# Kernel tuning notes

Hardware: AMD Instinct MI355X
Metric: run time of the kernel (lower is better)

## Reference

```python
import jax, jax.numpy as jnp
import numpy as np

B, T, D = 2, 1024, 1024
E, H, TOPK = 32, 256, 4
S, HS = 2, H * TOPK  # shared experts, shared hidden dim


def setup_inputs() -> dict:
    key = jax.random.key(0)
    ks = jax.random.split(key, 10)
    sc = 0.02
    return {
        "x": jax.random.normal(ks[0], (B, T, D), dtype=jnp.float32),
        "Wr": jax.random.normal(ks[1], (E, D), dtype=jnp.float32) * sc,
        "router_bias": jnp.zeros((E,), dtype=jnp.float32),
        "Wg": jax.random.normal(ks[2], (E, H, D), dtype=jnp.float32) * sc,
        "Wu": jax.random.normal(ks[3], (E, H, D), dtype=jnp.float32) * sc,
        "Wd": jax.random.normal(ks[4], (E, D, H), dtype=jnp.float32) * sc,
        "Sg": jax.random.normal(ks[5], (S, HS, D), dtype=jnp.float32) * sc,
        "Su": jax.random.normal(ks[6], (S, HS, D), dtype=jnp.float32) * sc,
        "Sd": jax.random.normal(ks[7], (S, D, HS), dtype=jnp.float32) * sc,
    }


def reference(x, Wr, router_bias, Wg, Wu, Wd, Sg, Su, Sd):
    Bx, Tx, Dx = x.shape
    flat = x.reshape(-1, Dx)                      # [N, D]
    N = flat.shape[0]

    # Router: softmax over raw logits, top-k selection on biased logits
    logits = flat @ Wr.T                          # [N, E]
    scores = jax.nn.softmax(logits, axis=-1)
    _, topk_idx = jax.lax.top_k(logits + router_bias, TOPK)   # [N, K]
    topk_scores = jnp.take_along_axis(scores, topk_idx, axis=-1)
    topk_scores = topk_scores / jnp.sum(topk_scores, axis=-1, keepdims=True)

    # Dense per-token per-expert combine weights (0 for unselected experts)
    cw = jnp.zeros((N, E), dtype=flat.dtype).at[
        jnp.arange(N)[:, None], topk_idx
    ].add(topk_scores)                            # [N, E]

    # Routed experts: SwiGLU applied per expert, zero-weighted if unselected
    g = jnp.einsum("nd,ehd->neh", flat, Wg)       # [N, E, H]
    u = jnp.einsum("nd,ehd->neh", flat, Wu)
    h = jax.nn.silu(g) * u
    hw = h * cw[:, :, None]                       # fold combine weight before down-proj
    out = jnp.einsum("neh,edh->nd", hw, Wd)       # [N, D]

    # Shared experts: always active, summed on top
    gs = jnp.einsum("nd,shd->nsh", flat, Sg)      # [N, S, HS]
    us = jnp.einsum("nd,shd->nsh", flat, Su)
    hs = jax.nn.silu(gs) * us
    out = out + jnp.einsum("nsh,sdh->nd", hs, Sd)

    return out.reshape(Bx, Tx, Dx)
```

## Files before the change

kernel.cpp:

```cpp
#include <hip/hip_runtime.h>
#include <hip/hip_bf16.h>


#define N_TOK 2048
#define DDIM 1024
#define NEXP 32
#define HDIM 256
#define TOPK 4
#define NSH 2
#define HSH 1024
#define CNTS 32
#define WMAX 160
#define WM2  96

typedef unsigned short us4 __attribute__((ext_vector_type(4)));
typedef unsigned short us8 __attribute__((ext_vector_type(8)));
typedef short bf16x8 __attribute__((ext_vector_type(8)));
typedef float f32x4 __attribute__((ext_vector_type(4)));

__device__ __forceinline__ unsigned short f2bf(float f) {
  union { float f; unsigned u; } v; v.f = f;
  unsigned r = v.u + 0x7fffu + ((v.u >> 16) & 1u);
  return (unsigned short)(r >> 16);
}
__device__ __forceinline__ float bf2f(unsigned short h) {
  union { unsigned u; float f; } v; v.u = ((unsigned)h) << 16; return v.f;
}
__device__ __forceinline__ uint2 cvt4u(float4 v) {
  union { __hip_bfloat162 b; unsigned u; } a, b2;
  a.b  = __float22bfloat162_rn(make_float2(v.x, v.y));
  b2.b = __float22bfloat162_rn(make_float2(v.z, v.w));
  return make_uint2(a.u, b2.u);
}

__device__ __forceinline__ void pipe_barrier() {
  asm volatile("s_waitcnt lgkmcnt(0)" ::: "memory");
  __builtin_amdgcn_s_barrier();
  __builtin_amdgcn_sched_barrier(0);
}

#define C_X4   524288L
#define C_WG4  2621440L
#define C_WU4  4718592L
#define C_WD4  6815744L
#define C_SG4  7340032L
#define C_SU4  7864320L
#define C_TOT4 8388608L
#define NCVT   16384

__global__ __launch_bounds__(256) void k_prep(const float* __restrict__ x,
                                              const float* __restrict__ Wr,
                                              const float* __restrict__ rb,
                                              const float* __restrict__ Wg,
                                              const float* __restrict__ Wu,
                                              const float* __restrict__ Wd,
                                              const float* __restrict__ Sg,
                                              const float* __restrict__ Su,
                                              const float* __restrict__ Sd,
                                              unsigned short* __restrict__ xb,
                                              unsigned short* __restrict__ Wgb,
                                              unsigned short* __restrict__ Wub,
                                              unsigned short* __restrict__ Wdb,
                                              unsigned short* __restrict__ Sgb,
                                              unsigned short* __restrict__ Sub,
                                              unsigned short* __restrict__ Sdb,
                                              int* __restrict__ cnt,
                                              int* __restrict__ ent,
                                              float* __restrict__ wgt) {
  __shared__ float sX[8 * 1024];
  __shared__ float sLog[8 * 32];
  int tid = threadIdx.x;
  if (blockIdx.x >= 256) {
    long base = (long)(blockIdx.x - 256) * 512;
    const float* s; unsigned short* d; long off;
    if (base < C_WG4) {
      if (base < C_X4)  { s = x;  d = xb;  off = base; }
      else              { s = Wg; d = Wgb; off = base - C_X4; }
    } else if (base < C_WD4) {
      if (base < C_WU4) { s = Wu; d = Wub; off = base - C_WG4; }
      else              { s = Wd; d = Wdb; off = base - C_WU4; }
    } else if (base < C_SU4) {
      if (base < C_SG4) { s = Sg; d = Sgb; off = base - C_WD4; }
      else              { s = Su; d = Sub; off = base - C_SG4; }
    } else              { s = Sd; d = Sdb; off = base - C_SU4; }
    long i0 = off + 2 * tid;
    float4 v0 = reinterpret_cast<const float4*>(s)[i0];
    float4 v1 = reinterpret_cast<const float4*>(s)[i0 + 1];
    uint2 a = cvt4u(v0), b = cvt4u(v1);
    uint4 o = make_uint4(a.x, a.y, b.x, b.y);
    reinterpret_cast<uint4*>(d)[(off >> 1) + tid] = o;
    return;
  }
  int blk = blockIdx.x;
  {
    const float4* xsrc = reinterpret_cast<const float4*>(x + (size_t)blk * 8 * 1024);
    float4* xdst = reinterpret_cast<float4*>(sX);
#pragma unroll
    for (int i = 0; i < 8; i++) xdst[tid + 256 * i] = xsrc[tid + 256 * i];
  }
  __syncthreads();
  int tloc = tid >> 5, e = tid & 31;
  const float4* wr4 = reinterpret_cast<const float4*>(Wr + (size_t)e * DDIM);
  const float* xr = sX + tloc * 1024;
  float acc = 0.f;
#pragma unroll 8
  for (int d4 = 0; d4 < 256; d4++) {
    float4 wv = wr4[d4];
    acc += xr[d4 * 4 + 0] * wv.x + xr[d4 * 4 + 1] * wv.y +
           xr[d4 * 4 + 2] * wv.z + xr[d4 * 4 + 3] * wv.w;
  }
  sLog[tloc * 32 + e] = acc;
  __syncthreads();
  if (tid < 8) {
    int tok = blk * 8 + tid;
    const float* lg = sLog + tid * 32;
    int usedmask = 0;
    int idx[TOPK]; float lv[TOPK];
#pragma unroll
    for (int k = 0; k < TOPK; k++) {
      float best = -3.4e38f; int bi = 0;
      for (int ee = 0; ee < NEXP; ee++) {
        if ((usedmask >> ee) & 1) continue;
        float v = lg[ee] + rb[ee];
        if (v > best) { best = v; bi = ee; }
      }
      usedmask |= 1 << bi; idx[k] = bi; lv[k] = lg[bi];
    }
    float m = fmaxf(fmaxf(lv[0], lv[1]), fmaxf(lv[2], lv[3]));
    float w[TOPK]; float ssum = 0.f;
#pragma unroll
    for (int k = 0; k < TOPK; k++) { w[k] = __expf(lv[k] - m); ssum += w[k]; }
    float inv = 1.f / ssum;
#pragma unroll
    for (int k = 0; k < TOPK; k++) {
      int ee = idx[k];
      int pos = atomicAdd(&cnt[ee * CNTS], 1);
      ent[ee * N_TOK + pos] = tok * TOPK + k;
      wgt[ee * N_TOK + pos] = w[k] * inv;
    }
  }
}

__global__ void k_plan(const int* __restrict__ cnt, int* __restrict__ wk, int* __restrict__ nwk,
                       int* __restrict__ wk2, int* __restrict__ nwk2) {
  if (threadIdx.x != 0) return;
  int w = 0, w2 = 0;
  for (int e = 0; e < NEXP; e++) {
    int ne = cnt[e * CNTS];
    int nt = (ne + 63) >> 6;
    for (int t = 0; t < nt; t++) wk[w++] = e | (t << 8);
    int nt2 = (ne + 127) >> 7;
    for (int t = 0; t < nt2; t++) wk2[w2++] = e | (t << 8);
  }
  nwk[0] = w;
  nwk2[0] = w2;
}

__global__ __launch_bounds__(512) void k_routed_gu(const unsigned short* __restrict__ xb,
                                                   const unsigned short* __restrict__ Wgb,
                                                   const unsigned short* __restrict__ Wub,
                                                   const int* __restrict__ cnt,
                                                   const int* __restrict__ ent,
                                                   const float* __restrict__ wgt,
                                                   unsigned short* __restrict__ hw,
                                                   const int* __restrict__ wk2,
                                                   const int* __restrict__ nwk2) {
  int widx = blockIdx.x;
  if (widx >= nwk2[0]) return;
  int item = wk2[widx];
  int e = item & 255, mt = item >> 8, ht = blockIdx.y;
  int ne = cnt[e * CNTS];
  __shared__ unsigned short sA[2][128 * 40];
  __shared__ unsigned short sB[2][128 * 40];
  __shared__ int sTok[128];
  __shared__ float sW[128];
  int tid = threadIdx.x, lane = tid & 63, wid = tid >> 6;
  int wm = wid >> 2, wn = wid & 3;
  if (tid < 128) {
    int pos = mt * 128 + tid;
    int p2 = min(pos, ne - 1);
    sTok[tid] = ent[e * N_TOK + p2];
    sW[tid] = (pos < ne) ? wgt[e * N_TOK + p2] : 0.f;
  }
  __syncthreads();

  int ar = tid >> 2, akc = tid & 3;
  const unsigned short* aSrc = xb + (size_t)(sTok[ar] >> 2) * DDIM + akc * 8;
  int aOff = ar * 40 + akc * 8;
  int br = tid >> 2, bkc = tid & 3;
  int sel = (br >> 4) & 1;
  int h = ht * 64 + ((br >> 5) << 4) + (br & 15);
  const unsigned short* bSrc = (sel ? Wub : Wgb) + (size_t)(e * HDIM + h) * DDIM + bkc * 8;
  int bOff = br * 40 + bkc * 8;

  us8 aReg = *reinterpret_cast<const us8*>(aSrc);
  us8 bReg = *reinterpret_cast<const us8*>(bSrc);

  f32x4 acc[4][2];
#pragma unroll
  for (int mf = 0; mf < 4; mf++)
#pragma unroll
    for (int nf = 0; nf < 2; nf++) acc[mf][nf] = {0.f, 0.f, 0.f, 0.f};

  int cur = 0;
  for (int step = 0; step < 32; ++step) {
    *reinterpret_cast<us8*>(&sA[cur][aOff]) = aReg;
    *reinterpret_cast<us8*>(&sB[cur][bOff]) = bReg;
    if (step < 31) {
      int k0 = (step + 1) * 32;
      aReg = *reinterpret_cast<const us8*>(aSrc + k0);
      bReg = *reinterpret_cast<const us8*>(bSrc + k0);
    }
    pipe_barrier();
    int ka = (lane >> 4) * 8;
    bf16x8 a[4];
#pragma unroll
    for (int mf = 0; mf < 4; mf++)
      a[mf] = *reinterpret_cast<const bf16x8*>(&sA[cur][(wm * 64 + mf * 16 + (lane & 15)) * 40 + ka]);
#pragma unroll
    for (int nf = 0; nf < 2; nf++) {
      bf16x8 b = *reinterpret_cast<const bf16x8*>(&sB[cur][(wn * 32 + nf * 16 + (lane & 15)) * 40 + ka]);
#pragma unroll
      for (int mf = 0; mf < 4; mf++)
        acc[mf][nf] = __builtin_amdgcn_mfma_f32_16x16x32_bf16(a[mf], b, acc[mf][nf], 0, 0, 0);
    }
    cur ^= 1;
  }
#pragma unroll
  for (int mf = 0; mf < 4; mf++) {
#pragma unroll
    for (int r = 0; r < 4; r++) {
      int tl = wm * 64 + mf * 16 + ((lane >> 4) << 2) + r;
      int pos = mt * 128 + tl;
      if (pos < ne) {
        float g = acc[mf][0][r], u = acc[mf][1][r];
        float hval = (g / (1.f + __expf(-g))) * u * sW[tl];
        int ts = sTok[tl];
        int hcol = ht * 64 + wn * 16 + (lane & 15);
        hw[(size_t)ts * HDIM + hcol] = f2bf(hval);
      }
    }
  }
}

__global__ __launch_bounds__(512) void k_routed_down(const unsigned short* __restrict__ hw,
                                                     const unsigned short* __restrict__ Wdb,
                                                     const int* __restrict__ cnt,
                                                     const int* __restrict__ ent,
                                                     unsigned short* __restrict__ Pslot,
                                                     const int* __restrict__ wk2,
                                                     const int* __restrict__ nwk2) {
  int widx = blockIdx.x;
  if (widx >= nwk2[0]) return;
  int item = wk2[widx];
  int e = item & 255, mt = item >> 8, dh = blockIdx.y;
  int ne = cnt[e * CNTS];
  __shared__ unsigned short sA[2][128 * 40];
  __shared__ unsigned short sB[2][128 * 40];
  __shared__ int sTok[128];
  int tid = threadIdx.x, lane = tid & 63, wid = tid >> 6;
  int wm = wid >> 2, wn = wid & 3;
  if (tid < 128) {
    int pos = mt * 128 + tid;
    int p2 = min(pos, ne - 1);
    sTok[tid] = ent[e * N_TOK + p2];
  }
  __syncthreads();

  int ar = tid >> 2, akc = tid & 3;
  const unsigned short* aSrc = hw + (size_t)sTok[ar] * HDIM + akc * 8;
  int aOff = ar * 40 + akc * 8;
  int br = tid >> 2, bkc = tid & 3;
  int d0 = dh * 128 + br;
  const unsigned short* bSrc = Wdb + (size_t)(e * DDIM + d0) * HDIM + bkc * 8;
  int bOff = br * 40 + bkc * 8;

  us8 aReg = *reinterpret_cast<const us8*>(aSrc);
  us8 bReg = *reinterpret_cast<const us8*>(bSrc);

  f32x4 acc[4][2];
#pragma unroll
  for (int mf = 0; mf < 4; mf++)
#pragma unroll
    for (int nf = 0; nf < 2; nf++) acc[mf][nf] = {0.f, 0.f, 0.f, 0.f};

  int cur = 0;
  for (int step = 0; step < 8; ++step) {
    *reinterpret_cast<us8*>(&sA[cur][aOff]) = aReg;
    *reinterpret_cast<us8*>(&sB[cur][bOff]) = bReg;
    if (step < 7) {
      int k0 = (step + 1) * 32;
      aReg = *reinterpret_cast<const us8*>(aSrc + k0);
      bReg = *reinterpret_cast<const us8*>(bSrc + k0);
    }
    pipe_barrier();
    int ka = (lane >> 4) * 8;
    bf16x8 a[4];
#pragma unroll
    for (int mf = 0; mf < 4; mf++)
      a[mf] = *reinterpret_cast<const bf16x8*>(&sA[cur][(wm * 64 + mf * 16 + (lane & 15)) * 40 + ka]);
#pragma unroll
    for (int nf = 0; nf < 2; nf++) {
      bf16x8 b = *reinterpret_cast<const bf16x8*>(&sB[cur][(wn * 32 + nf * 16 + (lane & 15)) * 40 + ka]);
#pragma unroll
      for (int mf = 0; mf < 4; mf++)
        acc[mf][nf] = __builtin_amdgcn_mfma_f32_16x16x32_bf16(a[mf], b, acc[mf][nf], 0, 0, 0);
    }
    cur ^= 1;
  }
#pragma unroll
  for (int mf = 0; mf < 4; mf++) {
#pragma unroll
    for (int nf = 0; nf < 2; nf++) {
#pragma unroll
      for (int r = 0; r < 4; r++) {
        int tl = wm * 64 + mf * 16 + ((lane >> 4) << 2) + r;
        int pos = mt * 128 + tl;
        if (pos < ne) {
          int ts = sTok[tl];
          int d = dh * 128 + wn * 32 + nf * 16 + (lane & 15);
          Pslot[(size_t)ts * DDIM + d] = f2bf(acc[mf][nf][r]);
        }
      }
    }
  }
}

__global__ __launch_bounds__(512) void k_shared_gu(const unsigned short* __restrict__ xb,
                                                   const unsigned short* __restrict__ Sgb,
                                                   const unsigned short* __restrict__ Sub,
                                                   unsigned short* __restrict__ hs) {
  int s = blockIdx.x >> 3, ht = blockIdx.x & 7;
  int mt = blockIdx.y;
  __shared__ unsigned short sA[2][128 * 40];
  __shared__ unsigned short sB[2][256 * 40];
  int tid = threadIdx.x, lane = tid & 63, wid = tid >> 6;
  int wm = wid >> 2, wn = wid & 3;

  int ar = tid >> 2, akc = tid & 3;
  const unsigned short* aSrc = xb + (size_t)(mt * 128 + ar) * DDIM + akc * 8;
  int aOff = ar * 40 + akc * 8;
  const unsigned short* bSrc[2];
  int bOff[2];
#pragma unroll
  for (int p = 0; p < 2; p++) {
    int c = tid + p * 512;
    int row = c >> 2, kc = c & 3;
    int sel = (row >> 4) & 1;
    int h = ht * 128 + ((row >> 5) << 4) + (row & 15);
    bSrc[p] = (sel ? Sub : Sgb) + (size_t)(s * HSH + h) * DDIM + kc * 8;
    bOff[p] = row * 40 + kc * 8;
  }

  us8 aReg = *reinterpret_cast<const us8*>(aSrc);
  us8 bReg[2];
#pragma unroll
  for (int p = 0; p < 2; p++) bReg[p] = *reinterpret_cast<const us8*>(bSrc[p]);

  f32x4 acc[4][4];
#pragma unroll
  for (int mf = 0; mf < 4; mf++)
#pragma unroll
    for (int nf = 0; nf < 4; nf++) acc[mf][nf] = {0.f, 0.f, 0.f, 0.f};

  int cur = 0;
  for (int step = 0; step < 32; ++step) {
    *reinterpret_cast<us8*>(&sA[cur][aOff]) = aReg;
#pragma unroll
    for (int p = 0; p < 2; p++) *reinterpret_cast<us8*>(&sB[cur][bOff[p]]) = bReg[p];
    if (step < 31) {
      int k0 = (step + 1) * 32;
      aReg = *reinterpret_cast<const us8*>(aSrc + k0);
#pragma unroll
      for (int p = 0; p < 2; p++) bReg[p] = *reinterpret_cast<const us8*>(bSrc[p] + k0);
    }
    pipe_barrier();
    int ka = (lane >> 4) * 8;
    bf16x8 a[4];
#pragma unroll
    for (int mf = 0; mf < 4; mf++)
      a[mf] = *reinterpret_cast<const bf16x8*>(&sA[cur][(wm * 64 + mf * 16 + (lane & 15)) * 40 + ka]);
#pragma unroll
    for (int nf = 0; nf < 4; nf++) {
      bf16x8 b = *reinterpret_cast<const bf16x8*>(&sB[cur][(wn * 64 + nf * 16 + (lane & 15)) * 40 + ka]);
#pragma unroll
      for (int mf = 0; mf < 4; mf++)
        acc[mf][nf] = __builtin_amdgcn_mfma_f32_16x16x32_bf16(a[mf], b, acc[mf][nf], 0, 0, 0);
    }
    cur ^= 1;
  }
#pragma unroll
  for (int mf = 0; mf < 4; mf++) {
#pragma unroll
    for (int t = 0; t < 2; t++) {
#pragma unroll
      for (int r = 0; r < 4; r++) {
        int tok = mt * 128 + wm * 64 + mf * 16 + ((lane >> 4) << 2) + r;
        float g = acc[mf][2 * t][r], u = acc[mf][2 * t + 1][r];
        float hval = (g / (1.f + __expf(-g))) * u;
        int h = ht * 128 + (wn * 2 + t) * 16 + (lane & 15);
        hs[(size_t)(tok * NSH + s) * HSH + h] = f2bf(hval);
      }
    }
  }
}

__global__ __launch_bounds__(512) void k_shared_down(const unsigned short* __restrict__ hs,
                                                     const unsigned short* __restrict__ Sdb,
                                                     unsigned short* __restrict__ Psh) {
  int dh = blockIdx.x >> 1, s = blockIdx.x & 1;
  int mt = blockIdx.y;
  __shared__ unsigned short sA[2][128 * 40];
  __shared__ unsigned short sB[2][128 * 40];
  int tid = threadIdx.x, lane = tid & 63, wid = tid >> 6;
  int wm = wid >> 2, wn = wid & 3;

  int ar = tid >> 2, akc = tid & 3;
  const unsigned short* aSrc = hs + (size_t)((mt * 128 + ar) * NSH + s) * HSH + akc * 8;
  int aOff = ar * 40 + akc * 8;
  int br = tid >> 2, bkc = tid & 3;
  const unsigned short* bSrc = Sdb + (size_t)(s * DDIM + dh * 128 + br) * HSH + bkc * 8;
  int bOff = br * 40 + bkc * 8;

  us8 aReg = *reinterpret_cast<const us8*>(aSrc);
  us8 bReg = *reinterpret_cast<const us8*>(bSrc);

  f32x4 acc[4][2];
#pragma unroll
  for (int mf = 0; mf < 4; mf++)
#pragma unroll
    for (int nf = 0; nf < 2; nf++) acc[mf][nf] = {0.f, 0.f, 0.f, 0.f};

  int cur = 0;
  for (int step = 0; step < 32; ++step) {
    *reinterpret_cast<us8*>(&sA[cur][aOff]) = aReg;
    *reinterpret_cast<us8*>(&sB[cur][bOff]) = bReg;
    if (step < 31) {
      int k0 = (step + 1) * 32;
      aReg = *reinterpret_cast<const us8*>(aSrc + k0);
      bReg = *reinterpret_cast<const us8*>(bSrc + k0);
    }
    pipe_barrier();
    int ka = (lane >> 4) * 8;
    bf16x8 a[4];
#pragma unroll
    for (int mf = 0; mf < 4; mf++)
      a[mf] = *reinterpret_cast<const bf16x8*>(&sA[cur][(wm * 64 + mf * 16 + (lane & 15)) * 40 + ka]);
#pragma unroll
    for (int nf = 0; nf < 2; nf++) {
      bf16x8 b = *reinterpret_cast<const bf16x8*>(&sB[cur][(wn * 32 + nf * 16 + (lane & 15)) * 40 + ka]);
#pragma unroll
      for (int mf = 0; mf < 4; mf++)
        acc[mf][nf] = __builtin_amdgcn_mfma_f32_16x16x32_bf16(a[mf], b, acc[mf][nf], 0, 0, 0);
    }
    cur ^= 1;
  }
#pragma unroll
  for (int mf = 0; mf < 4; mf++) {
#pragma unroll
    for (int nf = 0; nf < 2; nf++) {
#pragma unroll
      for (int r = 0; r < 4; r++) {
        int tok = mt * 128 + wm * 64 + mf * 16 + ((lane >> 4) << 2) + r;
        int d = dh * 128 + wn * 32 + nf * 16 + (lane & 15);
        Psh[(size_t)s * N_TOK * DDIM + (size_t)tok * DDIM + d] = f2bf(acc[mf][nf][r]);
      }
    }
  }
}

__global__ __launch_bounds__(256) void k_combine(const unsigned short* __restrict__ Pslot,
                                                 const unsigned short* __restrict__ Psh,
                                                 float* __restrict__ out) {
  int i = blockIdx.x * 256 + threadIdx.x;
  int base = i * 8;
  int tok = base >> 10, d = base & 1023;
  const us8 p0 = *reinterpret_cast<const us8*>(Pslot + ((size_t)tok * 4 + 0) * DDIM + d);
  const us8 p1 = *reinterpret_cast<const us8*>(Pslot + ((size_t)tok * 4 + 1) * DDIM + d);
  const us8 p2 = *reinterpret_cast<const us8*>(Pslot + ((size_t)tok * 4 + 2) * DDIM + d);
  const us8 p3 = *reinterpret_cast<const us8*>(Pslot + ((size_t)tok * 4 + 3) * DDIM + d);
  const us8 q0 = *reinterpret_cast<const us8*>(Psh + (size_t)base);
  const us8 q1 = *reinterpret_cast<const us8*>(Psh + (size_t)N_TOK * DDIM + base);
  float o[8];
#pragma unroll
  for (int j = 0; j < 8; j++)
    o[j] = bf2f(p0[j]) + bf2f(p1[j]) + bf2f(p2[j]) + bf2f(p3[j]) + bf2f(q0[j]) + bf2f(q1[j]);
  float4 v0 = {o[0], o[1], o[2], o[3]};
  float4 v1 = {o[4], o[5], o[6], o[7]};
  reinterpret_cast<float4*>(out + base)[0] = v0;
  reinterpret_cast<float4*>(out + base)[1] = v1;
}

extern "C" void kernel_launch(void* const* d_in, const int* in_sizes, int n_in,
                              void* d_out, int out_size, void* d_ws, size_t ws_size,
                              hipStream_t stream) {
  const float* x  = (const float*)d_in[0];
  const float* Wr = (const float*)d_in[1];
  const float* rb = (const float*)d_in[2];
  const float* Wg = (const float*)d_in[3];
  const float* Wu = (const float*)d_in[4];
  const float* Wd = (const float*)d_in[5];
  const float* Sg = (const float*)d_in[6];
  const float* Su = (const float*)d_in[7];
  const float* Sd = (const float*)d_in[8];
  float* out = (float*)d_out;
  char* w = (char*)d_ws;

  unsigned short* xb    = (unsigned short*)(w + (size_t)0);
  unsigned short* Wgb   = (unsigned short*)(w + ((size_t)4  << 20));
  unsigned short* Wub   = (unsigned short*)(w + ((size_t)20 << 20));
  unsigned short* Wdb   = (unsigned short*)(w + ((size_t)36 << 20));
  unsigned short* Sgb   = (unsigned short*)(w + ((size_t)52 << 20));
  unsigned short* Sub   = (unsigned short*)(w + ((size_t)56 << 20));
  unsigned short* Sdb   = (unsigned short*)(w + ((size_t)60 << 20));
  unsigned short* hw    = (unsigned short*)(w + ((size_t)64 << 20));
  unsigned short* hs    = (unsigned short*)(w + ((size_t)68 << 20));
  unsigned short* Pslot = (unsigned short*)(w + ((size_t)76 << 20));
  unsigned short* Psh   = (unsigned short*)(w + ((size_t)92 << 20));
  int*   cnt = (int*)(w + ((size_t)100 << 20));
  int*   ent = (int*)(w + ((size_t)100 << 20) + 8192);
  float* wgt = (float*)(w + ((size_t)100 << 20) + 8192 + (size_t)NEXP * N_TOK * 4);
  int*   wk   = (int*)(w + ((size_t)102 << 20));
  int*   nwk  = (int*)(w + ((size_t)102 << 20) + 4096);
  int*   wk2  = (int*)(w + ((size_t)102 << 20) + 8192);
  int*   nwk2 = (int*)(w + ((size_t)102 << 20) + 12288);

  hipMemsetAsync(cnt, 0, NEXP * CNTS * sizeof(int), stream);

  k_prep<<<256 + NCVT, 256, 0, stream>>>(x, Wr, rb, Wg, Wu, Wd, Sg, Su, Sd,
                                         xb, Wgb, Wub, Wdb, Sgb, Sub, Sdb,
                                         cnt, ent, wgt);
  k_plan<<<1, 64, 0, stream>>>(cnt, wk, nwk, wk2, nwk2);

  k_routed_gu<<<dim3(WM2, 4), 512, 0, stream>>>(xb, Wgb, Wub, cnt, ent, wgt, hw, wk2, nwk2);
  k_routed_down<<<dim3(WM2, 8), 512, 0, stream>>>(hw, Wdb, cnt, ent, Pslot, wk2, nwk2);

  k_shared_gu<<<dim3(16, 16), 512, 0, stream>>>(xb, Sgb, Sub, hs);
  k_shared_down<<<dim3(16, 16), 512, 0, stream>>>(hs, Sdb, Psh);

  k_combine<<<N_TOK * DDIM / (256 * 8), 256, 0, stream>>>(Pslot, Psh, out);
}
```

Measured before the change: 161.9 us.

## Merge shared and routed expert GEMMs into combined launches; parallelize plan

Combines the shared-expert and routed-expert gate/up GEMMs into one kernel, and likewise the two down-projection GEMMs, by dispatching on block index. Shared blocks come first and routed work items follow. This cuts the launch count from four GEMM kernels to two and lets shared and routed tiles run together to fill the GPU. The plan kernel now builds its work list with a wave-wide shuffle prefix over experts instead of a serial loop, and the unused 64-row list is dropped. The cost is a larger shared-memory pool per block, sized for the bigger shared tile, which may lower occupancy for the routed blocks.

```diff
diff --git a/kernel.cpp b/kernel.cpp
--- a/kernel.cpp
+++ b/kernel.cpp
@@ -10,7 +10,6 @@
 #define NSH 2
 #define HSH 1024
 #define CNTS 32
-#define WMAX 160
 #define WM2  96
 
 typedef unsigned short us4 __attribute__((ext_vector_type(4)));
@@ -141,41 +140,122 @@
   }
 }
 
-__global__ void k_plan(const int* __restrict__ cnt, int* __restrict__ wk, int* __restrict__ nwk,
-                       int* __restrict__ wk2, int* __restrict__ nwk2) {
-  if (threadIdx.x != 0) return;
-  int w = 0, w2 = 0;
-  for (int e = 0; e < NEXP; e++) {
-    int ne = cnt[e * CNTS];
-    int nt = (ne + 63) >> 6;
-    for (int t = 0; t < nt; t++) wk[w++] = e | (t << 8);
-    int nt2 = (ne + 127) >> 7;
-    for (int t = 0; t < nt2; t++) wk2[w2++] = e | (t << 8);
-  }
-  nwk[0] = w;
-  nwk2[0] = w2;
-}
-
-__global__ __launch_bounds__(512) void k_routed_gu(const unsigned short* __restrict__ xb,
-                                                   const unsigned short* __restrict__ Wgb,
-                                                   const unsigned short* __restrict__ Wub,
-                                                   const int* __restrict__ cnt,
-                                                   const int* __restrict__ ent,
-                                                   const float* __restrict__ wgt,
-                                                   unsigned short* __restrict__ hw,
-                                                   const int* __restrict__ wk2,
-                                                   const int* __restrict__ nwk2) {
-  int widx = blockIdx.x;
-  if (widx >= nwk2[0]) return;
-  int item = wk2[widx];
-  int e = item & 255, mt = item >> 8, ht = blockIdx.y;
+__global__ void k_plan(const int* __restrict__ cnt, int* __restrict__ wk2, int* __restrict__ nwk2) {
+  int e = threadIdx.x;
+  if (e >= 32) return;
   int ne = cnt[e * CNTS];
-  __shared__ unsigned short sA[2][128 * 40];
-  __shared__ unsigned short sB[2][128 * 40];
+  int nt2 = (ne + 127) >> 7;
+  int off2 = 0;
+  for (int j = 0; j < 32; j++) {
+    int v2 = __shfl(nt2, j);
+    if (j < e) off2 += v2;
+  }
+  for (int t = 0; t < nt2; t++) wk2[off2 + t] = e | (t << 8);
+  if (e == 31) nwk2[0] = off2 + nt2;
+}
+
+__global__ __launch_bounds__(512) void k_gu(const unsigned short* __restrict__ xb,
+                                            const unsigned short* __restrict__ Sgb,
+                                            const unsigned short* __restrict__ Sub,
+                                            const unsigned short* __restrict__ Wgb,
+                                            const unsigned short* __restrict__ Wub,
+                                            const int* __restrict__ cnt,
+                                            const int* __restrict__ ent,
+                                            const float* __restrict__ wgt,
+                                            unsigned short* __restrict__ hs,
+                                            unsigned short* __restrict__ hw,
+                                            const int* __restrict__ wk2,
+                                            const int* __restrict__ nwk2) {
+  __shared__ unsigned short sPool[2 * 128 * 40 + 2 * 256 * 40];
   __shared__ int sTok[128];
   __shared__ float sW[128];
   int tid = threadIdx.x, lane = tid & 63, wid = tid >> 6;
   int wm = wid >> 2, wn = wid & 3;
+  int b = blockIdx.x;
+
+  if (b < 256) {
+    int xg = b & 15, mt = b >> 4;
+    int s = xg >> 3, ht = xg & 7;
+    unsigned short* sA = sPool;
+    unsigned short* sB = sPool + 2 * 128 * 40;
+
+    int ar = tid >> 2, akc = tid & 3;
+    const unsigned short* aSrc = xb + (size_t)(mt * 128 + ar) * DDIM + akc * 8;
+    int aOff = ar * 40 + akc * 8;
+    const unsigned short* bSrc[2];
+    int bOff[2];
+#pragma unroll
+    for (int p = 0; p < 2; p++) {
+      int c = tid + p * 512;
+      int row = c >> 2, kc = c & 3;
+      int sel = (row >> 4) & 1;
+      int h = ht * 128 + ((row >> 5) << 4) + (row & 15);
+      bSrc[p] = (sel ? Sub : Sgb) + (size_t)(s * HSH + h) * DDIM + kc * 8;
+      bOff[p] = row * 40 + kc * 8;
+    }
+
+    us8 aReg = *reinterpret_cast<const us8*>(aSrc);
+    us8 bReg[2];
+#pragma unroll
+    for (int p = 0; p < 2; p++) bReg[p] = *reinterpret_cast<const us8*>(bSrc[p]);
+
+    f32x4 acc[4][4];
+#pragma unroll
+    for (int mf = 0; mf < 4; mf++)
+#pragma unroll
+      for (int nf = 0; nf < 4; nf++) acc[mf][nf] = {0.f, 0.f, 0.f, 0.f};
+
+    int cur = 0;
+    for (int step = 0; step < 32; ++step) {
+      *reinterpret_cast<us8*>(&sA[cur * 5120 + aOff]) = aReg;
+#pragma unroll
+      for (int p = 0; p < 2; p++) *reinterpret_cast<us8*>(&sB[cur * 10240 + bOff[p]]) = bReg[p];
+      if (step < 31) {
+        int k0 = (step + 1) * 32;
+        aReg = *reinterpret_cast<const us8*>(aSrc + k0);
+#pragma unroll
+        for (int p = 0; p < 2; p++) bReg[p] = *reinterpret_cast<const us8*>(bSrc[p] + k0);
+      }
+      pipe_barrier();
+      int ka = (lane >> 4) * 8;
+      bf16x8 a[4];
+#pragma unroll
+      for (int mf = 0; mf < 4; mf++)
+        a[mf] = *reinterpret_cast<const bf16x8*>(&sA[cur * 5120 + (wm * 64 + mf * 16 + (lane & 15)) * 40 + ka]);
+#pragma unroll
+      for (int nf = 0; nf < 4; nf++) {
+        bf16x8 bb = *reinterpret_cast<const bf16x8*>(&sB[cur * 10240 + (wn * 64 + nf * 16 + (lane & 15)) * 40 + ka]);
+#pragma unroll
+        for (int mf = 0; mf < 4; mf++)
+          acc[mf][nf] = __builtin_amdgcn_mfma_f32_16x16x32_bf16(a[mf], bb, acc[mf][nf], 0, 0, 0);
+      }
+      cur ^= 1;
+    }
+#pragma unroll
+    for (int mf = 0; mf < 4; mf++) {
+#pragma unroll
+      for (int t = 0; t < 2; t++) {
+#pragma unroll
+        for (int r = 0; r < 4; r++) {
+          int tok = mt * 128 + wm * 64 + mf * 16 + ((lane >> 4) << 2) + r;
+          float g = acc[mf][2 * t][r], u = acc[mf][2 * t + 1][r];
+          float hval = (g / (1.f + __expf(-g))) * u;
+          int h = ht * 128 + (wn * 2 + t) * 16 + (lane & 15);
+          hs[(size_t)(tok * NSH + s) * HSH + h] = f2bf(hval);
+        }
+      }
+    }
+    return;
+  }
+
+  int idx = b - 256;
+  int widx = idx >> 2, ht = idx & 3;
+  if (widx >= nwk2[0]) return;
+  int item = wk2[widx];
+  int e = item & 255, mt = item >> 8;
+  int ne = cnt[e * CNTS];
+  unsigned short* sA = sPool;
+  unsigned short* sB = sPool + 2 * 128 * 40;
   if (tid < 128) {
     int pos = mt * 128 + tid;
     int p2 = min(pos, ne - 1);
@@ -204,8 +284,8 @@
 
   int cur = 0;
   for (int step = 0; step < 32; ++step) {
-    *reinterpret_cast<us8*>(&sA[cur][aOff]) = aReg;
-    *reinterpret_cast<us8*>(&sB[cur][bOff]) = bReg;
+    *reinterpret_cast<us8*>(&sA[cur * 5120 + aOff]) = aReg;
+    *reinterpret_cast<us8*>(&sB[cur * 5120 + bOff]) = bReg;
     if (step < 31) {
       int k0 = (step + 1) * 32;
       aReg = *reinterpret_cast<const us8*>(aSrc + k0);
@@ -216,13 +296,13 @@
     bf16x8 a[4];
 #pragma unroll
     for (int mf = 0; mf < 4; mf++)
-      a[mf] = *reinterpret_cast<const bf16x8*>(&sA[cur][(wm * 64 + mf * 16 + (lane & 15)) * 40 + ka]);
+      a[mf] = *reinterpret_cast<const bf16x8*>(&sA[cur * 5120 + (wm * 64 + mf * 16 + (lane & 15)) * 40 + ka]);
 #pragma unroll
     for (int nf = 0; nf < 2; nf++) {
-      bf16x8 b = *reinterpret_cast<const bf16x8*>(&sB[cur][(wn * 32 + nf * 16 + (lane & 15)) * 40 + ka]);
+      bf16x8 bb = *reinterpret_cast<const bf16x8*>(&sB[cur * 5120 + (wn * 32 + nf * 16 + (lane & 15)) * 40 + ka]);
 #pragma unroll
       for (int mf = 0; mf < 4; mf++)
-        acc[mf][nf] = __builtin_amdgcn_mfma_f32_16x16x32_bf16(a[mf], b, acc[mf][nf], 0, 0, 0);
+        acc[mf][nf] = __builtin_amdgcn_mfma_f32_16x16x32_bf16(a[mf], bb, acc[mf][nf], 0, 0, 0);
     }
     cur ^= 1;
   }
@@ -243,23 +323,89 @@
   }
 }
 
-__global__ __launch_bounds__(512) void k_routed_down(const unsigned short* __restrict__ hw,
-                                                     const unsigned short* __restrict__ Wdb,
-                                                     const int* __restrict__ cnt,
-                                                     const int* __restrict__ ent,
-                                                     unsigned short* __restrict__ Pslot,
-                                                     const int* __restrict__ wk2,
-                                                     const int* __restrict__ nwk2) {
-  int widx = blockIdx.x;
-  if (widx >= nwk2[0]) return;
-  int item = wk2[widx];
-  int e = item & 255, mt = item >> 8, dh = blockIdx.y;
-  int ne = cnt[e * CNTS];
-  __shared__ unsigned short sA[2][128 * 40];
-  __shared__ unsigned short sB[2][128 * 40];
+__global__ __launch_bounds__(512) void k_down(const unsigned short* __restrict__ hs,
+                                              const unsigned short* __restrict__ Sdb,
+                                              const unsigned short* __restrict__ hw,
+                                              const unsigned short* __restrict__ Wdb,
+                                              const int* __restrict__ cnt,
+                                              const int* __restrict__ ent,
+                                              unsigned short* __restrict__ Psh,
+                                              unsigned short* __restrict__ Pslot,
+                                              const int* __restrict__ wk2,
+                                              const int* __restrict__ nwk2) {
+  __shared__ unsigned short sPool[4 * 128 * 40];
   __shared__ int sTok[128];
   int tid = threadIdx.x, lane = tid & 63, wid = tid >> 6;
   int wm = wid >> 2, wn = wid & 3;
+  int b = blockIdx.x;
+  unsigned short* sA = sPool;
+  unsigned short* sB = sPool + 2 * 128 * 40;
+
+  if (b < 256) {
+    int xg = b & 15, mt = b >> 4;
+    int dh = xg >> 1, s = xg & 1;
+
+    int ar = tid >> 2, akc = tid & 3;
+    const unsigned short* aSrc = hs + (size_t)((mt * 128 + ar) * NSH + s) * HSH + akc * 8;
+    int aOff = ar * 40 + akc * 8;
+    int br = tid >> 2, bkc = tid & 3;
+    const unsigned short* bSrc = Sdb + (size_t)(s * DDIM + dh * 128 + br) * HSH + bkc * 8;
+    int bOff = br * 40 + bkc * 8;
+
+    us8 aReg = *reinterpret_cast<const us8*>(aSrc);
+    us8 bReg = *reinterpret_cast<const us8*>(bSrc);
+
+    f32x4 acc[4][2];
+#pragma unroll
+    for (int mf = 0; mf < 4; mf++)
+#pragma unroll
+      for (int nf = 0; nf < 2; nf++) acc[mf][nf] = {0.f, 0.f, 0.f, 0.f};
+
+    int cur = 0;
+    for (int step = 0; step < 32; ++step) {
+      *reinterpret_cast<us8*>(&sA[cur * 5120 + aOff]) = aReg;
+      *reinterpret_cast<us8*>(&sB[cur * 5120 + bOff]) = bReg;
+      if (step < 31) {
+        int k0 = (step + 1) * 32;
+        aReg = *reinterpret_cast<const us8*>(aSrc + k0);
+        bReg = *reinterpret_cast<const us8*>(bSrc + k0);
+      }
+      pipe_barrier();
+      int ka = (lane >> 4) * 8;
+      bf16x8 a[4];
+#pragma unroll
+      for (int mf = 0; mf < 4; mf++)
+        a[mf] = *reinterpret_cast<const bf16x8*>(&sA[cur * 5120 + (wm * 64 + mf * 16 + (lane & 15)) * 40 + ka]);
+#pragma unroll
+      for (int nf = 0; nf < 2; nf++) {
+        bf16x8 bb = *reinterpret_cast<const bf16x8*>(&sB[cur * 5120 + (wn * 32 + nf * 16 + (lane & 15)) * 40 + ka]);
+#pragma unroll
+        for (int mf = 0; mf < 4; mf++)
+          acc[mf][nf] = __builtin_amdgcn_mfma_f32_16x16x32_bf16(a[mf], bb, acc[mf][nf], 0, 0, 0);
+      }
+      cur ^= 1;
+    }
+#pragma unroll
+    for (int mf = 0; mf < 4; mf++) {
+#pragma unroll
+      for (int nf = 0; nf < 2; nf++) {
+#pragma unroll
+        for (int r = 0; r < 4; r++) {
+          int tok = mt * 128 + wm * 64 + mf * 16 + ((lane >> 4) << 2) + r;
+          int d = dh * 128 + wn * 32 + nf * 16 + (lane & 15);
+          Psh[(size_t)s * N_TOK * DDIM + (size_t)tok * DDIM + d] = f2bf(acc[mf][nf][r]);
+        }
+      }
+    }
+    return;
+  }
+
+  int idx = b - 256;
+  int widx = idx >> 3, dh = idx & 7;
+  if (widx >= nwk2[0]) return;
+  int item = wk2[widx];
+  int e = item & 255, mt = item >> 8;
+  int ne = cnt[e * CNTS];
   if (tid < 128) {
     int pos = mt * 128 + tid;
     int p2 = min(pos, ne - 1);
@@ -286,8 +432,8 @@
 
   int cur = 0;
   for (int step = 0; step < 8; ++step) {
-    *reinterpret_cast<us8*>(&sA[cur][aOff]) = aReg;
-    *reinterpret_cast<us8*>(&sB[cur][bOff]) = bReg;
+    *reinterpret_cast<us8*>(&sA[cur * 5120 + aOff]) = aReg;
+    *reinterpret_cast<us8*>(&sB[cur * 5120 + bOff]) = bReg;
     if (step < 7) {
       int k0 = (step + 1) * 32;
       aReg = *reinterpret_cast<const us8*>(aSrc + k0);
@@ -298,13 +444,13 @@
     bf16x8 a[4];
 #pragma unroll
     for (int mf = 0; mf < 4; mf++)
-      a[mf] = *reinterpret_cast<const bf16x8*>(&sA[cur][(wm * 64 + mf * 16 + (lane & 15)) * 40 + ka]);
+      a[mf] = *reinterpret_cast<const bf16x8*>(&sA[cur * 5120 + (wm * 64 + mf * 16 + (lane & 15)) * 40 + ka]);
 #pragma unroll
     for (int nf = 0; nf < 2; nf++) {
-      bf16x8 b = *reinterpret_cast<const bf16x8*>(&sB[cur][(wn * 32 + nf * 16 + (lane & 15)) * 40 + ka]);
+      bf16x8 bb = *reinterpret_cast<const bf16x8*>(&sB[cur * 5120 + (wn * 32 + nf * 16 + (lane & 15)) * 40 + ka]);
 #pragma unroll
       for (int mf = 0; mf < 4; mf++)
-        acc[mf][nf] = __builtin_amdgcn_mfma_f32_16x16x32_bf16(a[mf], b, acc[mf][nf], 0, 0, 0);
+        acc[mf][nf] = __builtin_amdgcn_mfma_f32_16x16x32_bf16(a[mf], bb, acc[mf][nf], 0, 0, 0);
     }
     cur ^= 1;
   }
@@ -321,149 +467,6 @@
           int d = dh * 128 + wn * 32 + nf * 16 + (lane & 15);
           Pslot[(size_t)ts * DDIM + d] = f2bf(acc[mf][nf][r]);
         }
-      }
-    }
-  }
-}
-
-__global__ __launch_bounds__(512) void k_shared_gu(const unsigned short* __restrict__ xb,
-                                                   const unsigned short* __restrict__ Sgb,
-                                                   const unsigned short* __restrict__ Sub,
-                                                   unsigned short* __restrict__ hs) {
-  int s = blockIdx.x >> 3, ht = blockIdx.x & 7;
-  int mt = blockIdx.y;
-  __shared__ unsigned short sA[2][128 * 40];
-  __shared__ unsigned short sB[2][256 * 40];
-  int tid = threadIdx.x, lane = tid & 63, wid = tid >> 6;
-  int wm = wid >> 2, wn = wid & 3;
-
-  int ar = tid >> 2, akc = tid & 3;
-  const unsigned short* aSrc = xb + (size_t)(mt * 128 + ar) * DDIM + akc * 8;
-  int aOff = ar * 40 + akc * 8;
-  const unsigned short* bSrc[2];
-  int bOff[2];
-#pragma unroll
-  for (int p = 0; p < 2; p++) {
-    int c = tid + p * 512;
-    int row = c >> 2, kc = c & 3;
-    int sel = (row >> 4) & 1;
-    int h = ht * 128 + ((row >> 5) << 4) + (row & 15);
-    bSrc[p] = (sel ? Sub : Sgb) + (size_t)(s * HSH + h) * DDIM + kc * 8;
-    bOff[p] = row * 40 + kc * 8;
-  }
-
-  us8 aReg = *reinterpret_cast<const us8*>(aSrc);
-  us8 bReg[2];
-#pragma unroll
-  for (int p = 0; p < 2; p++) bReg[p] = *reinterpret_cast<const us8*>(bSrc[p]);
-
-  f32x4 acc[4][4];
-#pragma unroll
-  for (int mf = 0; mf < 4; mf++)
-#pragma unroll
-    for (int nf = 0; nf < 4; nf++) acc[mf][nf] = {0.f, 0.f, 0.f, 0.f};
-
-  int cur = 0;
-  for (int step = 0; step < 32; ++step) {
-    *reinterpret_cast<us8*>(&sA[cur][aOff]) = aReg;
-#pragma unroll
-    for (int p = 0; p < 2; p++) *reinterpret_cast<us8*>(&sB[cur][bOff[p]]) = bReg[p];
-    if (step < 31) {
-      int k0 = (step + 1) * 32;
-      aReg = *reinterpret_cast<const us8*>(aSrc + k0);
-#pragma unroll
-      for (int p = 0; p < 2; p++) bReg[p] = *reinterpret_cast<const us8*>(bSrc[p] + k0);
-    }
-    pipe_barrier();
-    int ka = (lane >> 4) * 8;
-    bf16x8 a[4];
-#pragma unroll
-    for (int mf = 0; mf < 4; mf++)
-      a[mf] = *reinterpret_cast<const bf16x8*>(&sA[cur][(wm * 64 + mf * 16 + (lane & 15)) * 40 + ka]);
-#pragma unroll
-    for (int nf = 0; nf < 4; nf++) {
-      bf16x8 b = *reinterpret_cast<const bf16x8*>(&sB[cur][(wn * 64 + nf * 16 + (lane & 15)) * 40 + ka]);
-#pragma unroll
-      for (int mf = 0; mf < 4; mf++)
-        acc[mf][nf] = __builtin_amdgcn_mfma_f32_16x16x32_bf16(a[mf], b, acc[mf][nf], 0, 0, 0);
-    }
-    cur ^= 1;
-  }
-#pragma unroll
-  for (int mf = 0; mf < 4; mf++) {
-#pragma unroll
-    for (int t = 0; t < 2; t++) {
-#pragma unroll
-      for (int r = 0; r < 4; r++) {
-        int tok = mt * 128 + wm * 64 + mf * 16 + ((lane >> 4) << 2) + r;
-        float g = acc[mf][2 * t][r], u = acc[mf][2 * t + 1][r];
-        float hval = (g / (1.f + __expf(-g))) * u;
-        int h = ht * 128 + (wn * 2 + t) * 16 + (lane & 15);
-        hs[(size_t)(tok * NSH + s) * HSH + h] = f2bf(hval);
-      }
-    }
-  }
-}
-
-__global__ __launch_bounds__(512) void k_shared_down(const unsigned short* __restrict__ hs,
-                                                     const unsigned short* __restrict__ Sdb,
-                                                     unsigned short* __restrict__ Psh) {
-  int dh = blockIdx.x >> 1, s = blockIdx.x & 1;
-  int mt = blockIdx.y;
-  __shared__ unsigned short sA[2][128 * 40];
-  __shared__ unsigned short sB[2][128 * 40];
-  int tid = threadIdx.x, lane = tid & 63, wid = tid >> 6;
-  int wm = wid >> 2, wn = wid & 3;
-
-  int ar = tid >> 2, akc = tid & 3;
-  const unsigned short* aSrc = hs + (size_t)((mt * 128 + ar) * NSH + s) * HSH + akc * 8;
-  int aOff = ar * 40 + akc * 8;
-  int br = tid >> 2, bkc = tid & 3;
-  const unsigned short* bSrc = Sdb + (size_t)(s * DDIM + dh * 128 + br) * HSH + bkc * 8;
-  int bOff = br * 40 + bkc * 8;
-
-  us8 aReg = *reinterpret_cast<const us8*>(aSrc);
-  us8 bReg = *reinterpret_cast<const us8*>(bSrc);
-
-  f32x4 acc[4][2];
-#pragma unroll
-  for (int mf = 0; mf < 4; mf++)
-#pragma unroll
-    for (int nf = 0; nf < 2; nf++) acc[mf][nf] = {0.f, 0.f, 0.f, 0.f};
-
-  int cur = 0;
-  for (int step = 0; step < 32; ++step) {
-    *reinterpret_cast<us8*>(&sA[cur][aOff]) = aReg;
-    *reinterpret_cast<us8*>(&sB[cur][bOff]) = bReg;
-    if (step < 31) {
-      int k0 = (step + 1) * 32;
-      aReg = *reinterpret_cast<const us8*>(aSrc + k0);
-      bReg = *reinterpret_cast<const us8*>(bSrc + k0);
-    }
-    pipe_barrier();
-    int ka = (lane >> 4) * 8;
-    bf16x8 a[4];
-#pragma unroll
-    for (int mf = 0; mf < 4; mf++)
-      a[mf] = *reinterpret_cast<const bf16x8*>(&sA[cur][(wm * 64 + mf * 16 + (lane & 15)) * 40 + ka]);
-#pragma unroll
-    for (int nf = 0; nf < 2; nf++) {
-      bf16x8 b = *reinterpret_cast<const bf16x8*>(&sB[cur][(wn * 32 + nf * 16 + (lane & 15)) * 40 + ka]);
-#pragma unroll
-      for (int mf = 0; mf < 4; mf++)
-        acc[mf][nf] = __builtin_amdgcn_mfma_f32_16x16x32_bf16(a[mf], b, acc[mf][nf], 0, 0, 0);
-    }
-    cur ^= 1;
-  }
-#pragma unroll
-  for (int mf = 0; mf < 4; mf++) {
-#pragma unroll
-    for (int nf = 0; nf < 2; nf++) {
-#pragma unroll
-      for (int r = 0; r < 4; r++) {
-        int tok = mt * 128 + wm * 64 + mf * 16 + ((lane >> 4) << 2) + r;
-        int d = dh * 128 + wn * 32 + nf * 16 + (lane & 15);
-        Psh[(size_t)s * N_TOK * DDIM + (size_t)tok * DDIM + d] = f2bf(acc[mf][nf][r]);
       }
     }
   }
@@ -520,23 +523,20 @@
   int*   cnt = (int*)(w + ((size_t)100 << 20));
   int*   ent = (int*)(w + ((size_t)100 << 20) + 8192);
   float* wgt = (float*)(w + ((size_t)100 << 20) + 8192 + (size_t)NEXP * N_TOK * 4);
-  int*   wk   = (int*)(w + ((size_t)102 << 20));
-  int*   nwk  = (int*)(w + ((size_t)102 << 20) + 4096);
-  int*   wk2  = (int*)(w + ((size_t)102 << 20) + 8192);
-  int*   nwk2 = (int*)(w + ((size_t)102 << 20) + 12288);
+  int*   wk2  = (int*)(w + ((size_t)102 << 20));
+  int*   nwk2 = (int*)(w + ((size_t)102 << 20) + 4096);
 
   hipMemsetAsync(cnt, 0, NEXP * CNTS * sizeof(int), stream);
 
   k_prep<<<256 + NCVT, 256, 0, stream>>>(x, Wr, rb, Wg, Wu, Wd, Sg, Su, Sd,
                                          xb, Wgb, Wub, Wdb, Sgb, Sub, Sdb,
                                          cnt, ent, wgt);
-  k_plan<<<1, 64, 0, stream>>>(cnt, wk, nwk, wk2, nwk2);
-
-  k_routed_gu<<<dim3(WM2, 4), 512, 0, stream>>>(xb, Wgb, Wub, cnt, ent, wgt, hw, wk2, nwk2);
-  k_routed_down<<<dim3(WM2, 8), 512, 0, stream>>>(hw, Wdb, cnt, ent, Pslot, wk2, nwk2);
-
-  k_shared_gu<<<dim3(16, 16), 512, 0, stream>>>(xb, Sgb, Sub, hs);
-  k_shared_down<<<dim3(16, 16), 512, 0, stream>>>(hs, Sdb, Psh);
+  k_plan<<<1, 64, 0, stream>>>(cnt, wk2, nwk2);
+
+  k_gu<<<256 + WM2 * 4, 512, 0, stream>>>(xb, Sgb, Sub, Wgb, Wub, cnt, ent, wgt,
+                                          hs, hw, wk2, nwk2);
+  k_down<<<256 + WM2 * 8, 512, 0, stream>>>(hs, Sdb, hw, Wdb, cnt, ent,
+                                            Psh, Pslot, wk2, nwk2);
 
   k_combine<<<N_TOK * DDIM / (256 * 8), 256, 0, stream>>>(Pslot, Psh, out);
 }
```

Result: faster. 136.9 us (median of 2 runs) (-15.4%).
